# Optimization experiments

Hardware: AMD Instinct MI355X
Metric: run time of the kernel (lower is better)

Reference implementation:

```python
import jax, jax.numpy as jnp
import numpy as np

N = 20000      # nodes
E = 320000     # edges (before self-loops)
G = 64         # graphs in batch
IN = 128       # input_dim
HID = 64       # hidden_dim
H1 = 4         # heads of conv1
NEG_SLOPE = 0.2


def setup_inputs() -> dict:
    key = jax.random.key(0)
    ks = jax.random.split(key, 14)
    x = jax.random.normal(ks[0], (N, IN), jnp.float32)
    edge_index = jax.random.randint(ks[1], (2, E), 0, N, dtype=jnp.int32)
    batch = jnp.sort(jax.random.randint(ks[2], (N,), 0, G, dtype=jnp.int32))
    # conv1: in=IN, out=HID, heads=4, concat
    W1 = jax.random.normal(ks[3], (IN, H1 * HID), jnp.float32) / np.float32(np.sqrt(IN))
    a_src1 = jax.random.normal(ks[4], (H1, HID), jnp.float32) / np.float32(np.sqrt(HID))
    a_dst1 = jax.random.normal(ks[5], (H1, HID), jnp.float32) / np.float32(np.sqrt(HID))
    b1 = jnp.zeros((H1 * HID,), jnp.float32)
    # conv2: in=4*HID, out=HID, heads=1
    W2 = jax.random.normal(ks[6], (H1 * HID, HID), jnp.float32) / np.float32(np.sqrt(H1 * HID))
    a_src2 = jax.random.normal(ks[7], (1, HID), jnp.float32) / np.float32(np.sqrt(HID))
    a_dst2 = jax.random.normal(ks[8], (1, HID), jnp.float32) / np.float32(np.sqrt(HID))
    b2 = jnp.zeros((HID,), jnp.float32)
    # final linear HID -> 1
    W_lin = jax.random.normal(ks[9], (HID, 1), jnp.float32) / np.float32(np.sqrt(HID))
    b_lin = jnp.zeros((1,), jnp.float32)
    return dict(x=x, edge_index=edge_index, batch=batch,
                W1=W1, a_src1=a_src1, a_dst1=a_dst1, b1=b1,
                W2=W2, a_src2=a_src2, a_dst2=a_dst2, b2=b2,
                W_lin=W_lin, b_lin=b_lin)


def gat_conv(x, src, dst, W, a_src, a_dst, b, heads, out_ch, n_nodes):
    """PyG-style GATConv (v1), concat=True, with self-loops already in src/dst."""
    h = (x @ W).reshape(n_nodes, heads, out_ch)          # [N,H,C]
    s = jnp.einsum('nhc,hc->nh', h, a_src)               # [N,H] per-node src score
    d = jnp.einsum('nhc,hc->nh', h, a_dst)               # [N,H] per-node dst score
    logits = jax.nn.leaky_relu(s[src] + d[dst], NEG_SLOPE)   # [Etot,H]
    # segment softmax over incoming edges of each destination node
    m = jax.ops.segment_max(logits, dst, num_segments=n_nodes)
    m = jnp.where(jnp.isfinite(m), m, 0.0)
    e = jnp.exp(logits - m[dst])                         # [Etot,H]
    denom = jax.ops.segment_sum(e, dst, num_segments=n_nodes)
    alpha = e / denom[dst]                               # every node has a self-loop -> denom>0
    out = jax.ops.segment_sum(alpha[:, :, None] * h[src], dst, num_segments=n_nodes)  # [N,H,C]
    return out.reshape(n_nodes, heads * out_ch) + b


def reference(x, edge_index, batch,
              W1, a_src1, a_dst1, b1,
              W2, a_src2, a_dst2, b2,
              W_lin, b_lin):
    n = x.shape[0]
    loop = jnp.arange(n, dtype=edge_index.dtype)
    src = jnp.concatenate([edge_index[0], loop])   # add self-loops (PyG default)
    dst = jnp.concatenate([edge_index[1], loop])
    h = jax.nn.elu(gat_conv(x, src, dst, W1, a_src1, a_dst1, b1, H1, HID, n))
    h = jax.nn.elu(gat_conv(h, src, dst, W2, a_src2, a_dst2, b2, 1, HID, n))
    # global mean pool over graphs
    sums = jax.ops.segment_sum(h, batch, num_segments=G)                 # [G,HID]
    cnt = jax.ops.segment_sum(jnp.ones((n,), h.dtype), batch, num_segments=G)
    pooled = sums / jnp.maximum(cnt, 1.0)[:, None]
    return (pooled @ W_lin + b_lin).squeeze(-1)    # [G]
```

## Files before the change

### kernel.cpp

```cpp
#include <hip/hip_runtime.h>
#include <cstdint>


__device__ __forceinline__ float leaky02(float x) { return x > 0.f ? x : 0.2f * x; }
__device__ __forceinline__ float eluf(float x) { return x > 0.f ? x : expm1f(x); }

template <int H>
__device__ __forceinline__ void sgemm_scores_body(
    const float* __restrict__ A, const float* __restrict__ B, float* __restrict__ C,
    int M, int K, const float* __restrict__ asrc, const float* __restrict__ adst,
    float* __restrict__ sT, float* __restrict__ dS, float* __restrict__ wself,
    int bx, int by, float* As_, float* Bs_) {
    constexpr int Nc = H * 64;
    float (*As)[68] = (float(*)[68])As_;
    float (*Bs)[68] = (float(*)[68])Bs_;
    const int tid = threadIdx.x;
    const int bm = bx * 64, bn = by * 64;
    const int ty = tid >> 4, tx = tid & 15;
    float acc[4][4] = {};
    for (int k0 = 0; k0 < K; k0 += 32) {
#pragma unroll
        for (int i = 0; i < 8; i++) {
            int idx = tid + i * 256;
            int m = idx >> 5, kk = idx & 31;
            int gm = bm + m;
            if (gm >= M) gm = 0;
            As[kk][m] = A[(size_t)gm * K + k0 + kk];
        }
#pragma unroll
        for (int i = 0; i < 8; i++) {
            int idx = tid + i * 256;
            int kk = idx >> 6, n = idx & 63;
            Bs[kk][n] = B[(size_t)(k0 + kk) * Nc + bn + n];
        }
        __syncthreads();
#pragma unroll
        for (int kk = 0; kk < 32; kk++) {
            float4 a4 = *(const float4*)&As[kk][ty * 4];
            float4 b4 = *(const float4*)&Bs[kk][tx * 4];
            float av[4] = {a4.x, a4.y, a4.z, a4.w};
            float bv[4] = {b4.x, b4.y, b4.z, b4.w};
#pragma unroll
            for (int r = 0; r < 4; r++)
#pragma unroll
                for (int c2 = 0; c2 < 4; c2++) acc[r][c2] += av[r] * bv[c2];
        }
        __syncthreads();
    }
    const int h = by;
    float sr[4], dr[4];
#pragma unroll
    for (int r = 0; r < 4; r++) {
        float s = 0.f, d = 0.f;
#pragma unroll
        for (int c2 = 0; c2 < 4; c2++) {
            float hv = acc[r][c2];
            s += hv * asrc[h * 64 + tx * 4 + c2];
            d += hv * adst[h * 64 + tx * 4 + c2];
        }
        sr[r] = s;
        dr[r] = d;
    }
#pragma unroll
    for (int off = 1; off <= 8; off <<= 1) {
#pragma unroll
        for (int r = 0; r < 4; r++) {
            sr[r] += __shfl_xor(sr[r], off);
            dr[r] += __shfl_xor(dr[r], off);
        }
    }
#pragma unroll
    for (int r = 0; r < 4; r++) {
        int gm = bm + ty * 4 + r;
        if (gm < M) {
            float4 o = make_float4(acc[r][0], acc[r][1], acc[r][2], acc[r][3]);
            *(float4*)&C[(size_t)gm * Nc + bn + tx * 4] = o;
            if (tx == 0) {
                sT[(size_t)h * M + gm] = sr[r];
                dS[gm * H + h] = dr[r];
                wself[gm * H + h] = __expf(leaky02(sr[r] + dr[r]));
            }
        }
    }
}

__global__ __launch_bounds__(256) void fused_sgemm4_init_kernel(
    const float* __restrict__ A, const float* __restrict__ B, float* __restrict__ C,
    int M, int K, const float* __restrict__ asrc, const float* __restrict__ adst,
    float* __restrict__ sT, float* __restrict__ dS, float* __restrict__ wself,
    int GBX, int GB1, int4* __restrict__ initp, int colN4, int totN4) {
    __shared__ __align__(16) float As_[32][68];
    __shared__ __align__(16) float Bs_[32][68];
    const int b = blockIdx.x;
    if (b >= GB1) {
        int i = (b - GB1) * 256 + threadIdx.x;
        if (i < totN4)
            initp[i] = (i < colN4) ? make_int4(-1, -1, -1, -1) : make_int4(0, 0, 0, 0);
        return;
    }
    sgemm_scores_body<4>(A, B, C, M, K, asrc, adst, sT, dS, wself,
                         b % GBX, b / GBX, &As_[0][0], &Bs_[0][0]);
}

__global__ __launch_bounds__(256) void sgemm_scores1_kernel(
    const float* __restrict__ A, const float* __restrict__ B, float* __restrict__ C,
    int M, int K, const float* __restrict__ asrc, const float* __restrict__ adst,
    float* __restrict__ sT, float* __restrict__ dS, float* __restrict__ wself) {
    __shared__ __align__(16) float As_[32][68];
    __shared__ __align__(16) float Bs_[32][68];
    sgemm_scores_body<1>(A, B, C, M, K, asrc, adst, sT, dS, wself,
                         blockIdx.x, 0, &As_[0][0], &Bs_[0][0]);
}

__global__ void fill_kernel(const int* __restrict__ src, const int* __restrict__ dst,
                            int* __restrict__ cursor, int* __restrict__ col, int E) {
    int e = blockIdx.x * blockDim.x + threadIdx.x;
    if (e >= E) return;
    int d = dst[e];
    int p = atomicAdd(&cursor[d], 1);
    if (p < 64) col[(d << 6) + p] = src[e];
}

__global__ __launch_bounds__(256) void gat_agg4_kernel(
    const float* __restrict__ hbuf, const float* __restrict__ sT,
    const float* __restrict__ dsc, const float* __restrict__ wself,
    const int* __restrict__ cursor, const int* __restrict__ col,
    const float* __restrict__ bias, float* __restrict__ out, int N) {
    const int slice = blockIdx.x & 7;
    const int lane = threadIdx.x & 63;
    const int cq = lane & 7;
    const int vidx = (blockIdx.x >> 3) * 32 + (threadIdx.x >> 6) * 8 + (lane >> 3);
    const bool valid = vidx < N;
    const int v = min(vidx, N - 1);
    const int deg = min(cursor[v], 64);
    const int base = v << 6;
    const int cbase = slice * 32 + cq * 4;
    const int hh = slice >> 1;
    const float* __restrict__ sTh = sT + (size_t)hh * N;
    const char* __restrict__ hb = (const char*)hbuf + ((size_t)cbase << 2);
    const float dvh = dsc[v * 4 + hh];
    float ws = wself[v * 4 + hh];
    float den = ws;
    float4 hv = *(const float4*)(hb + ((unsigned)v << 10));
    float4 acc = make_float4(ws * hv.x, ws * hv.y, ws * hv.z, ws * hv.w);
    const int end4 = (deg + 3) & ~3;
    for (int j = 0; j < end4; j += 4) {
        int4 c4 = *(const int4*)&col[base + j];
        unsigned i0 = (unsigned)max(c4.x, 0), i1 = (unsigned)max(c4.y, 0);
        unsigned i2 = (unsigned)max(c4.z, 0), i3 = (unsigned)max(c4.w, 0);
        float4 h0 = *(const float4*)(hb + (i0 << 10));
        float4 h1 = *(const float4*)(hb + (i1 << 10));
        float4 h2 = *(const float4*)(hb + (i2 << 10));
        float4 h3 = *(const float4*)(hb + (i3 << 10));
        float w0 = (c4.x >= 0) ? __expf(leaky02(sTh[i0] + dvh)) : 0.f;
        float w1 = (c4.y >= 0) ? __expf(leaky02(sTh[i1] + dvh)) : 0.f;
        float w2 = (c4.z >= 0) ? __expf(leaky02(sTh[i2] + dvh)) : 0.f;
        float w3 = (c4.w >= 0) ? __expf(leaky02(sTh[i3] + dvh)) : 0.f;
        den += w0 + w1 + w2 + w3;
        acc.x += w0 * h0.x + w1 * h1.x + w2 * h2.x + w3 * h3.x;
        acc.y += w0 * h0.y + w1 * h1.y + w2 * h2.y + w3 * h3.y;
        acc.z += w0 * h0.z + w1 * h1.z + w2 * h2.z + w3 * h3.z;
        acc.w += w0 * h0.w + w1 * h1.w + w2 * h2.w + w3 * h3.w;
    }
    if (valid) {
        float4 b4 = *(const float4*)&bias[cbase];
        float inv = 1.f / den;
        float4 r;
        r.x = eluf(acc.x * inv + b4.x);
        r.y = eluf(acc.y * inv + b4.y);
        r.z = eluf(acc.z * inv + b4.z);
        r.w = eluf(acc.w * inv + b4.w);
        *(float4*)&out[(size_t)v * 256 + cbase] = r;
    }
}

__global__ __launch_bounds__(256) void gat_agg1_kernel(
    const float* __restrict__ hbuf, const float* __restrict__ sT,
    const float* __restrict__ dsc, const float* __restrict__ wself,
    const int* __restrict__ cursor, const int* __restrict__ col,
    const float* __restrict__ bias, const float* __restrict__ Wlin,
    float* __restrict__ pn0, float* __restrict__ pn1, int N) {
    const int slice = blockIdx.x & 1;
    const int lane = threadIdx.x & 63;
    const int cq = lane & 7;
    const int vidx = (blockIdx.x >> 1) * 32 + (threadIdx.x >> 6) * 8 + (lane >> 3);
    const bool valid = vidx < N;
    const int v = min(vidx, N - 1);
    const int deg = min(cursor[v], 64);
    const int base = v << 6;
    const int cbase = slice * 32 + cq * 4;
    const char* __restrict__ hb = (const char*)hbuf + ((size_t)cbase << 2);
    const float dv = dsc[v];
    float ws = wself[v];
    float den = ws;
    float4 hv = *(const float4*)(hb + ((unsigned)v << 8));
    float4 acc = make_float4(ws * hv.x, ws * hv.y, ws * hv.z, ws * hv.w);
    const int end4 = (deg + 3) & ~3;
    for (int j = 0; j < end4; j += 4) {
        int4 c4 = *(const int4*)&col[base + j];
        unsigned i0 = (unsigned)max(c4.x, 0), i1 = (unsigned)max(c4.y, 0);
        unsigned i2 = (unsigned)max(c4.z, 0), i3 = (unsigned)max(c4.w, 0);
        float4 h0 = *(const float4*)(hb + (i0 << 8));
        float4 h1 = *(const float4*)(hb + (i1 << 8));
        float4 h2 = *(const float4*)(hb + (i2 << 8));
        float4 h3 = *(const float4*)(hb + (i3 << 8));
        float w0 = (c4.x >= 0) ? __expf(leaky02(sT[i0] + dv)) : 0.f;
        float w1 = (c4.y >= 0) ? __expf(leaky02(sT[i1] + dv)) : 0.f;
        float w2 = (c4.z >= 0) ? __expf(leaky02(sT[i2] + dv)) : 0.f;
        float w3 = (c4.w >= 0) ? __expf(leaky02(sT[i3] + dv)) : 0.f;
        den += w0 + w1 + w2 + w3;
        acc.x += w0 * h0.x + w1 * h1.x + w2 * h2.x + w3 * h3.x;
        acc.y += w0 * h0.y + w1 * h1.y + w2 * h2.y + w3 * h3.y;
        acc.z += w0 * h0.z + w1 * h1.z + w2 * h2.z + w3 * h3.z;
        acc.w += w0 * h0.w + w1 * h1.w + w2 * h2.w + w3 * h3.w;
    }
    float4 b4 = *(const float4*)&bias[cbase];
    float4 wl = *(const float4*)&Wlin[cbase];
    float inv = 1.f / den;
    float p = eluf(acc.x * inv + b4.x) * wl.x + eluf(acc.y * inv + b4.y) * wl.y +
              eluf(acc.z * inv + b4.z) * wl.z + eluf(acc.w * inv + b4.w) * wl.w;
    p += __shfl_xor(p, 1);
    p += __shfl_xor(p, 2);
    p += __shfl_xor(p, 4);
    if (valid && cq == 0) (slice ? pn1 : pn0)[v] = p;
}

__global__ __launch_bounds__(64) void finalize_kernel(const float* __restrict__ pn0,
                                                      const float* __restrict__ pn1,
                                                      const int* __restrict__ batch,
                                                      const float* __restrict__ blin,
                                                      float* __restrict__ outp, int N, int G) {
    const int g = blockIdx.x;
    const int lane = threadIdx.x;
    int lo = 0, hi = N;
    while (lo < hi) { int mid = (lo + hi) >> 1; if (batch[mid] < g) lo = mid + 1; else hi = mid; }
    int lo2 = lo, hi2 = N;
    while (lo2 < hi2) { int mid = (lo2 + hi2) >> 1; if (batch[mid] < g + 1) lo2 = mid + 1; else hi2 = mid; }
    float s = 0.f;
    for (int i = lo + lane; i < hi2; i += 64) s += pn0[i] + pn1[i];
#pragma unroll
    for (int off = 32; off > 0; off >>= 1) s += __shfl_xor(s, off);
    if (lane == 0) {
        float cnt = (float)(hi2 - lo);
        outp[g] = s / fmaxf(cnt, 1.f) + blin[0];
    }
}

extern "C" void kernel_launch(void* const* d_in, const int* in_sizes, int n_in,
                              void* d_out, int out_size, void* d_ws, size_t ws_size,
                              hipStream_t stream) {
    const float* x      = (const float*)d_in[0];
    const int*   ei     = (const int*)d_in[1];
    const int*   batch  = (const int*)d_in[2];
    const float* W1     = (const float*)d_in[3];
    const float* a_src1 = (const float*)d_in[4];
    const float* a_dst1 = (const float*)d_in[5];
    const float* b1     = (const float*)d_in[6];
    const float* W2     = (const float*)d_in[7];
    const float* a_src2 = (const float*)d_in[8];
    const float* a_dst2 = (const float*)d_in[9];
    const float* b2     = (const float*)d_in[10];
    const float* Wlin   = (const float*)d_in[11];
    const float* blin   = (const float*)d_in[12];

    const int N = in_sizes[2];
    const int E = in_sizes[1] / 2;
    const int G = out_size;
    const int* src = ei;
    const int* dst = ei + E;

    char* ws = (char*)d_ws;
    size_t off = 0;
    auto carve = [&](size_t bytes) -> char* {
        char* p = ws + off;
        off = (off + bytes + 255) & ~(size_t)255;
        return p;
    };
    float* h1      = (float*)carve((size_t)N * 256 * 4);
    float* out1    = (float*)carve((size_t)N * 256 * 4);
    float* sT1     = (float*)carve((size_t)4 * N * 4);
    float* d1      = (float*)carve((size_t)N * 4 * 4);
    float* wself1  = (float*)carve((size_t)N * 4 * 4);
    float* sT2     = (float*)carve((size_t)N * 4);
    float* d2      = (float*)carve((size_t)N * 4);
    float* wself2  = (float*)carve((size_t)N * 4);
    int*   colcur  = (int*)carve(((size_t)N * 64 + N) * 4);
    float* pn0     = (float*)carve((size_t)N * 4);
    float* pn1     = (float*)carve((size_t)N * 4);
    float* h2      = h1;
    int* col = colcur;
    int* cursor = colcur + (size_t)N * 64;

    const int GBX = (N + 63) / 64;
    const int GB1 = GBX * 4;
    const int totN4 = (N * 64 + N) / 4;
    const int colN4 = N * 16;
    const int GBI = (totN4 + 255) / 256;

    fused_sgemm4_init_kernel<<<GB1 + GBI, 256, 0, stream>>>(
        x, W1, h1, N, 128, a_src1, a_dst1, sT1, d1, wself1,
        GBX, GB1, (int4*)colcur, colN4, totN4);
    fill_kernel<<<(E + 255) / 256, 256, 0, stream>>>(src, dst, cursor, col, E);

    const int nodeGroups32 = (N + 31) / 32;
    gat_agg4_kernel<<<8 * nodeGroups32, 256, 0, stream>>>(h1, sT1, d1, wself1, cursor, col,
                                                          b1, out1, N);
    sgemm_scores1_kernel<<<dim3(GBX, 1), 256, 0, stream>>>(
        out1, W2, h2, N, 256, a_src2, a_dst2, sT2, d2, wself2);
    gat_agg1_kernel<<<2 * nodeGroups32, 256, 0, stream>>>(h2, sT2, d2, wself2, cursor, col,
                                                          b2, Wlin, pn0, pn1, N);
    finalize_kernel<<<G, 64, 0, stream>>>(pn0, pn1, batch, blin, (float*)d_out, N, G);
}
```

Measured before the change: 133.2 us.

## Store projected features in bf16 and remap aggregation threads per head

```diff
diff --git a/kernel.cpp b/kernel.cpp
--- a/kernel.cpp
+++ b/kernel.cpp
@@ -1,14 +1,26 @@
 #include <hip/hip_runtime.h>
+#include <hip/hip_bf16.h>
 #include <cstdint>
 
 
 __device__ __forceinline__ float leaky02(float x) { return x > 0.f ? x : 0.2f * x; }
 __device__ __forceinline__ float eluf(float x) { return x > 0.f ? x : expm1f(x); }
+__device__ __forceinline__ float bf2f(unsigned short u) {
+    return __uint_as_float((unsigned)u << 16);
+}
+__device__ __forceinline__ unsigned short f2bf(float f) {
+    unsigned x = __float_as_uint(f);
+    return (unsigned short)((x + 0x7FFF + ((x >> 16) & 1)) >> 16);
+}
+__device__ __forceinline__ float4 cv4(ushort4 u) {
+    return make_float4(bf2f(u.x), bf2f(u.y), bf2f(u.z), bf2f(u.w));
+}
 
 template <int H>
 __device__ __forceinline__ void sgemm_scores_body(
-    const float* __restrict__ A, const float* __restrict__ B, float* __restrict__ C,
-    int M, int K, const float* __restrict__ asrc, const float* __restrict__ adst,
+    const float* __restrict__ A, const float* __restrict__ B,
+    unsigned short* __restrict__ C, int M, int K,
+    const float* __restrict__ asrc, const float* __restrict__ adst,
     float* __restrict__ sT, float* __restrict__ dS, float* __restrict__ wself,
     int bx, int by, float* As_, float* Bs_) {
     constexpr int Nc = H * 64;
@@ -73,8 +85,12 @@
     for (int r = 0; r < 4; r++) {
         int gm = bm + ty * 4 + r;
         if (gm < M) {
-            float4 o = make_float4(acc[r][0], acc[r][1], acc[r][2], acc[r][3]);
-            *(float4*)&C[(size_t)gm * Nc + bn + tx * 4] = o;
+            ushort4 o;
+            o.x = f2bf(acc[r][0]);
+            o.y = f2bf(acc[r][1]);
+            o.z = f2bf(acc[r][2]);
+            o.w = f2bf(acc[r][3]);
+            *(ushort4*)&C[(size_t)gm * Nc + bn + tx * 4] = o;
             if (tx == 0) {
                 sT[(size_t)h * M + gm] = sr[r];
                 dS[gm * H + h] = dr[r];
@@ -85,8 +101,9 @@
 }
 
 __global__ __launch_bounds__(256) void fused_sgemm4_init_kernel(
-    const float* __restrict__ A, const float* __restrict__ B, float* __restrict__ C,
-    int M, int K, const float* __restrict__ asrc, const float* __restrict__ adst,
+    const float* __restrict__ A, const float* __restrict__ B,
+    unsigned short* __restrict__ C, int M, int K,
+    const float* __restrict__ asrc, const float* __restrict__ adst,
     float* __restrict__ sT, float* __restrict__ dS, float* __restrict__ wself,
     int GBX, int GB1, int4* __restrict__ initp, int colN4, int totN4) {
     __shared__ __align__(16) float As_[32][68];
@@ -103,8 +120,9 @@
 }
 
 __global__ __launch_bounds__(256) void sgemm_scores1_kernel(
-    const float* __restrict__ A, const float* __restrict__ B, float* __restrict__ C,
-    int M, int K, const float* __restrict__ asrc, const float* __restrict__ adst,
+    const float* __restrict__ A, const float* __restrict__ B,
+    unsigned short* __restrict__ C, int M, int K,
+    const float* __restrict__ asrc, const float* __restrict__ adst,
     float* __restrict__ sT, float* __restrict__ dS, float* __restrict__ wself) {
     __shared__ __align__(16) float As_[32][68];
     __shared__ __align__(16) float Bs_[32][68];
@@ -122,111 +140,114 @@
 }
 
 __global__ __launch_bounds__(256) void gat_agg4_kernel(
-    const float* __restrict__ hbuf, const float* __restrict__ sT,
+    const unsigned short* __restrict__ h1, const float* __restrict__ sT,
     const float* __restrict__ dsc, const float* __restrict__ wself,
     const int* __restrict__ cursor, const int* __restrict__ col,
     const float* __restrict__ bias, float* __restrict__ out, int N) {
-    const int slice = blockIdx.x & 7;
+    const int slice = blockIdx.x & 3;
+    const int sub = (blockIdx.x >> 2) & 1;
+    const int vgrp = (blockIdx.x >> 3) * 2 + sub;
     const int lane = threadIdx.x & 63;
-    const int cq = lane & 7;
-    const int vidx = (blockIdx.x >> 3) * 32 + (threadIdx.x >> 6) * 8 + (lane >> 3);
+    const int cq = lane & 15;
+    const int vidx = vgrp * 16 + (threadIdx.x >> 6) * 4 + (lane >> 4);
     const bool valid = vidx < N;
     const int v = min(vidx, N - 1);
     const int deg = min(cursor[v], 64);
     const int base = v << 6;
-    const int cbase = slice * 32 + cq * 4;
-    const int hh = slice >> 1;
-    const float* __restrict__ sTh = sT + (size_t)hh * N;
-    const char* __restrict__ hb = (const char*)hbuf + ((size_t)cbase << 2);
-    const float dvh = dsc[v * 4 + hh];
-    float ws = wself[v * 4 + hh];
+    const int ch = slice * 64 + cq * 4;
+    const float* __restrict__ sTh = sT + (size_t)slice * N;
+    const unsigned short* __restrict__ hp = h1 + slice * 64 + cq * 4;
+    const float dvh = dsc[v * 4 + slice];
+    float ws = wself[v * 4 + slice];
     float den = ws;
-    float4 hv = *(const float4*)(hb + ((unsigned)v << 10));
+    float4 hv = cv4(*(const ushort4*)(hp + ((size_t)v << 8)));
     float4 acc = make_float4(ws * hv.x, ws * hv.y, ws * hv.z, ws * hv.w);
     const int end4 = (deg + 3) & ~3;
+    int4 c4 = *(const int4*)&col[base];
     for (int j = 0; j < end4; j += 4) {
-        int4 c4 = *(const int4*)&col[base + j];
-        unsigned i0 = (unsigned)max(c4.x, 0), i1 = (unsigned)max(c4.y, 0);
-        unsigned i2 = (unsigned)max(c4.z, 0), i3 = (unsigned)max(c4.w, 0);
-        float4 h0 = *(const float4*)(hb + (i0 << 10));
-        float4 h1 = *(const float4*)(hb + (i1 << 10));
-        float4 h2 = *(const float4*)(hb + (i2 << 10));
-        float4 h3 = *(const float4*)(hb + (i3 << 10));
-        float w0 = (c4.x >= 0) ? __expf(leaky02(sTh[i0] + dvh)) : 0.f;
-        float w1 = (c4.y >= 0) ? __expf(leaky02(sTh[i1] + dvh)) : 0.f;
-        float w2 = (c4.z >= 0) ? __expf(leaky02(sTh[i2] + dvh)) : 0.f;
-        float w3 = (c4.w >= 0) ? __expf(leaky02(sTh[i3] + dvh)) : 0.f;
+        int4 cc = c4;
+        c4 = *(const int4*)&col[base + j + 4];
+        unsigned i0 = (unsigned)max(cc.x, 0), i1 = (unsigned)max(cc.y, 0);
+        unsigned i2 = (unsigned)max(cc.z, 0), i3 = (unsigned)max(cc.w, 0);
+        float4 h0 = cv4(*(const ushort4*)(hp + ((size_t)i0 << 8)));
+        float4 h1v = cv4(*(const ushort4*)(hp + ((size_t)i1 << 8)));
+        float4 h2v = cv4(*(const ushort4*)(hp + ((size_t)i2 << 8)));
+        float4 h3v = cv4(*(const ushort4*)(hp + ((size_t)i3 << 8)));
+        float w0 = (cc.x >= 0) ? __expf(leaky02(sTh[i0] + dvh)) : 0.f;
+        float w1 = (cc.y >= 0) ? __expf(leaky02(sTh[i1] + dvh)) : 0.f;
+        float w2 = (cc.z >= 0) ? __expf(leaky02(sTh[i2] + dvh)) : 0.f;
+        float w3 = (cc.w >= 0) ? __expf(leaky02(sTh[i3] + dvh)) : 0.f;
         den += w0 + w1 + w2 + w3;
-        acc.x += w0 * h0.x + w1 * h1.x + w2 * h2.x + w3 * h3.x;
-        acc.y += w0 * h0.y + w1 * h1.y + w2 * h2.y + w3 * h3.y;
-        acc.z += w0 * h0.z + w1 * h1.z + w2 * h2.z + w3 * h3.z;
-        acc.w += w0 * h0.w + w1 * h1.w + w2 * h2.w + w3 * h3.w;
+        acc.x += w0 * h0.x + w1 * h1v.x + w2 * h2v.x + w3 * h3v.x;
+        acc.y += w0 * h0.y + w1 * h1v.y + w2 * h2v.y + w3 * h3v.y;
+        acc.z += w0 * h0.z + w1 * h1v.z + w2 * h2v.z + w3 * h3v.z;
+        acc.w += w0 * h0.w + w1 * h1v.w + w2 * h2v.w + w3 * h3v.w;
     }
     if (valid) {
-        float4 b4 = *(const float4*)&bias[cbase];
+        float4 b4 = *(const float4*)&bias[ch];
         float inv = 1.f / den;
         float4 r;
         r.x = eluf(acc.x * inv + b4.x);
         r.y = eluf(acc.y * inv + b4.y);
         r.z = eluf(acc.z * inv + b4.z);
         r.w = eluf(acc.w * inv + b4.w);
-        *(float4*)&out[(size_t)v * 256 + cbase] = r;
+        *(float4*)&out[(size_t)v * 256 + ch] = r;
     }
 }
 
 __global__ __launch_bounds__(256) void gat_agg1_kernel(
-    const float* __restrict__ hbuf, const float* __restrict__ sT,
+    const unsigned short* __restrict__ h2, const float* __restrict__ sT,
     const float* __restrict__ dsc, const float* __restrict__ wself,
     const int* __restrict__ cursor, const int* __restrict__ col,
     const float* __restrict__ bias, const float* __restrict__ Wlin,
-    float* __restrict__ pn0, float* __restrict__ pn1, int N) {
-    const int slice = blockIdx.x & 1;
+    float* __restrict__ pn, int N) {
     const int lane = threadIdx.x & 63;
-    const int cq = lane & 7;
-    const int vidx = (blockIdx.x >> 1) * 32 + (threadIdx.x >> 6) * 8 + (lane >> 3);
+    const int cq = lane & 15;
+    const int vidx = blockIdx.x * 16 + (threadIdx.x >> 6) * 4 + (lane >> 4);
     const bool valid = vidx < N;
     const int v = min(vidx, N - 1);
     const int deg = min(cursor[v], 64);
     const int base = v << 6;
-    const int cbase = slice * 32 + cq * 4;
-    const char* __restrict__ hb = (const char*)hbuf + ((size_t)cbase << 2);
+    const unsigned short* __restrict__ hp = h2 + cq * 4;
     const float dv = dsc[v];
     float ws = wself[v];
     float den = ws;
-    float4 hv = *(const float4*)(hb + ((unsigned)v << 8));
+    float4 hv = cv4(*(const ushort4*)(hp + ((size_t)v << 6)));
     float4 acc = make_float4(ws * hv.x, ws * hv.y, ws * hv.z, ws * hv.w);
     const int end4 = (deg + 3) & ~3;
+    int4 c4 = *(const int4*)&col[base];
     for (int j = 0; j < end4; j += 4) {
-        int4 c4 = *(const int4*)&col[base + j];
-        unsigned i0 = (unsigned)max(c4.x, 0), i1 = (unsigned)max(c4.y, 0);
-        unsigned i2 = (unsigned)max(c4.z, 0), i3 = (unsigned)max(c4.w, 0);
-        float4 h0 = *(const float4*)(hb + (i0 << 8));
-        float4 h1 = *(const float4*)(hb + (i1 << 8));
-        float4 h2 = *(const float4*)(hb + (i2 << 8));
-        float4 h3 = *(const float4*)(hb + (i3 << 8));
-        float w0 = (c4.x >= 0) ? __expf(leaky02(sT[i0] + dv)) : 0.f;
-        float w1 = (c4.y >= 0) ? __expf(leaky02(sT[i1] + dv)) : 0.f;
-        float w2 = (c4.z >= 0) ? __expf(leaky02(sT[i2] + dv)) : 0.f;
-        float w3 = (c4.w >= 0) ? __expf(leaky02(sT[i3] + dv)) : 0.f;
+        int4 cc = c4;
+        c4 = *(const int4*)&col[base + j + 4];
+        unsigned i0 = (unsigned)max(cc.x, 0), i1 = (unsigned)max(cc.y, 0);
+        unsigned i2 = (unsigned)max(cc.z, 0), i3 = (unsigned)max(cc.w, 0);
+        float4 h0 = cv4(*(const ushort4*)(hp + ((size_t)i0 << 6)));
+        float4 h1v = cv4(*(const ushort4*)(hp + ((size_t)i1 << 6)));
+        float4 h2v = cv4(*(const ushort4*)(hp + ((size_t)i2 << 6)));
+        float4 h3v = cv4(*(const ushort4*)(hp + ((size_t)i3 << 6)));
+        float w0 = (cc.x >= 0) ? __expf(leaky02(sT[i0] + dv)) : 0.f;
+        float w1 = (cc.y >= 0) ? __expf(leaky02(sT[i1] + dv)) : 0.f;
+        float w2 = (cc.z >= 0) ? __expf(leaky02(sT[i2] + dv)) : 0.f;
+        float w3 = (cc.w >= 0) ? __expf(leaky02(sT[i3] + dv)) : 0.f;
         den += w0 + w1 + w2 + w3;
-        acc.x += w0 * h0.x + w1 * h1.x + w2 * h2.x + w3 * h3.x;
-        acc.y += w0 * h0.y + w1 * h1.y + w2 * h2.y + w3 * h3.y;
-        acc.z += w0 * h0.z + w1 * h1.z + w2 * h2.z + w3 * h3.z;
-        acc.w += w0 * h0.w + w1 * h1.w + w2 * h2.w + w3 * h3.w;
-    }
-    float4 b4 = *(const float4*)&bias[cbase];
-    float4 wl = *(const float4*)&Wlin[cbase];
+        acc.x += w0 * h0.x + w1 * h1v.x + w2 * h2v.x + w3 * h3v.x;
+        acc.y += w0 * h0.y + w1 * h1v.y + w2 * h2v.y + w3 * h3v.y;
+        acc.z += w0 * h0.z + w1 * h1v.z + w2 * h2v.z + w3 * h3v.z;
+        acc.w += w0 * h0.w + w1 * h1v.w + w2 * h2v.w + w3 * h3v.w;
+    }
+    float4 b4 = *(const float4*)&bias[cq * 4];
+    float4 wl = *(const float4*)&Wlin[cq * 4];
     float inv = 1.f / den;
     float p = eluf(acc.x * inv + b4.x) * wl.x + eluf(acc.y * inv + b4.y) * wl.y +
               eluf(acc.z * inv + b4.z) * wl.z + eluf(acc.w * inv + b4.w) * wl.w;
     p += __shfl_xor(p, 1);
     p += __shfl_xor(p, 2);
     p += __shfl_xor(p, 4);
-    if (valid && cq == 0) (slice ? pn1 : pn0)[v] = p;
-}
-
-__global__ __launch_bounds__(64) void finalize_kernel(const float* __restrict__ pn0,
-                                                      const float* __restrict__ pn1,
+    p += __shfl_xor(p, 8);
+    if (valid && cq == 0) pn[v] = p;
+}
+
+__global__ __launch_bounds__(64) void finalize_kernel(const float* __restrict__ pn,
                                                       const int* __restrict__ batch,
                                                       const float* __restrict__ blin,
                                                       float* __restrict__ outp, int N, int G) {
@@ -237,7 +258,7 @@
     int lo2 = lo, hi2 = N;
     while (lo2 < hi2) { int mid = (lo2 + hi2) >> 1; if (batch[mid] < g + 1) lo2 = mid + 1; else hi2 = mid; }
     float s = 0.f;
-    for (int i = lo + lane; i < hi2; i += 64) s += pn0[i] + pn1[i];
+    for (int i = lo + lane; i < hi2; i += 64) s += pn[i];
 #pragma unroll
     for (int off = 32; off > 0; off >>= 1) s += __shfl_xor(s, off);
     if (lane == 0) {
@@ -276,8 +297,9 @@
         off = (off + bytes + 255) & ~(size_t)255;
         return p;
     };
-    float* h1      = (float*)carve((size_t)N * 256 * 4);
+    unsigned short* h1 = (unsigned short*)carve((size_t)N * 256 * 2);
     float* out1    = (float*)carve((size_t)N * 256 * 4);
+    unsigned short* h2 = (unsigned short*)carve((size_t)N * 64 * 2);
     float* sT1     = (float*)carve((size_t)4 * N * 4);
     float* d1      = (float*)carve((size_t)N * 4 * 4);
     float* wself1  = (float*)carve((size_t)N * 4 * 4);
@@ -285,9 +307,7 @@
     float* d2      = (float*)carve((size_t)N * 4);
     float* wself2  = (float*)carve((size_t)N * 4);
     int*   colcur  = (int*)carve(((size_t)N * 64 + N) * 4);
-    float* pn0     = (float*)carve((size_t)N * 4);
-    float* pn1     = (float*)carve((size_t)N * 4);
-    float* h2      = h1;
+    float* pn      = (float*)carve((size_t)N * 4);
     int* col = colcur;
     int* cursor = colcur + (size_t)N * 64;
 
@@ -307,7 +327,7 @@
                                                           b1, out1, N);
     sgemm_scores1_kernel<<<dim3(GBX, 1), 256, 0, stream>>>(
         out1, W2, h2, N, 256, a_src2, a_dst2, sT2, d2, wself2);
-    gat_agg1_kernel<<<2 * nodeGroups32, 256, 0, stream>>>(h2, sT2, d2, wself2, cursor, col,
-                                                          b2, Wlin, pn0, pn1, N);
-    finalize_kernel<<<G, 64, 0, stream>>>(pn0, pn1, batch, blin, (float*)d_out, N, G);
-}
+    gat_agg1_kernel<<<(N + 15) / 16, 256, 0, stream>>>(h2, sT2, d2, wself2, cursor, col,
+                                                       b2, Wlin, pn, N);
+    finalize_kernel<<<G, 64, 0, stream>>>(pn, batch, blin, (float*)d_out, N, G);
+}
```

Measured after the change: 125.3 us. -5.9%, faster.
